# Kernel tuning notes

Hardware: AMD Instinct MI355X
Metric: run time of the kernel (lower is better)

## Reference

```python
import jax, jax.numpy as jnp
import numpy as np

N = 65536   # total sentences
B = 8192    # number of bags (ragged scopes)
C = 1024    # class_dim
R = 100     # rel_num


def setup_inputs() -> dict:
    key = jax.random.key(0)
    k1, k2, k3, k4 = jax.random.split(key, 4)
    X = jax.random.normal(k1, (N, C), jnp.float32)            # post-fc1 sentence reps
    Constraints = jax.random.normal(k2, (R, C), jnp.float32)  # post-fc2 constraint reps
    W = jax.random.normal(k3, (R, C), jnp.float32) * 0.02     # classifier weight
    b = jnp.zeros((R,), jnp.float32)                           # classifier bias
    # ragged scopes: random cut points -> contiguous [start, end) per bag
    rng = np.random.default_rng(0)
    cuts = np.sort(rng.choice(np.arange(1, N), B - 1, replace=False))
    starts = np.concatenate([[0], cuts])
    ends = np.concatenate([cuts, [N]])
    X_Scope = jnp.asarray(np.stack([starts, ends], axis=1), jnp.int32)  # [B, 2]
    X_Rel = jax.random.randint(k4, (B,), 0, R, jnp.int32)               # [B]
    return dict(X=X, Constraints=Constraints, W=W, b=b, X_Scope=X_Scope, X_Rel=X_Rel)


def reference(X, Constraints, W, b, X_Scope, X_Rel):
    n, _ = X.shape
    nb = X_Scope.shape[0]
    # map each sentence to its (contiguous) bag via scope starts
    starts = X_Scope[:, 0]
    seg = jnp.searchsorted(starts, jnp.arange(n, dtype=starts.dtype), side='right') - 1  # [N]
    # per-sentence attention logit against its bag's relation constraint
    Con = Constraints[X_Rel]                                   # [B, C]
    scores = jnp.einsum('nc,nc->n', X, Con[seg])               # [N]
    # numerically-stable per-bag softmax
    m = jax.ops.segment_max(scores, seg, num_segments=nb)      # [B]
    e = jnp.exp(scores - m[seg])                               # [N]
    denom = jax.ops.segment_sum(e, seg, num_segments=nb)       # [B]
    w = e / denom[seg]                                         # [N]
    # attention-weighted bag pooling
    bag = jax.ops.segment_sum(w[:, None] * X, seg, num_segments=nb)  # [B, C]
    # classifier (dropout is identity at eval)
    return bag @ W.T + b                                       # [B, R]
```

## Files before the change

### kernel.cpp

```cpp
#include <hip/hip_runtime.h>
#include <math.h>

#define CDIM 1024
#define RDIM 100
#define NBAGS 8192
#define RPAD 112
#define BPB 16
#define NBLK (NBAGS / BPB)

typedef float floatx4 __attribute__((ext_vector_type(4)));
typedef short bf16x8 __attribute__((ext_vector_type(8)));

__device__ __forceinline__ float dot4(float4 a, float4 b) {
    return a.x * b.x + a.y * b.y + a.z * b.z + a.w * b.w;
}

__device__ __forceinline__ unsigned short f2bf(float f) {
    unsigned int u = __builtin_bit_cast(unsigned int, f);
    u += 0x7FFFu + ((u >> 16) & 1u);
    return (unsigned short)(u >> 16);
}

#define LOADROW(D0, D1, D2, D3, ri)                                          \
    {                                                                        \
        const float4* p_ = (const float4*)(X + (size_t)(ri) * CDIM);         \
        D0 = p_[lane];       D1 = p_[lane + 64];                             \
        D2 = p_[lane + 128]; D3 = p_[lane + 192];                            \
    }

#define COMPUTE_ROW(A0, A1, A2, A3)                                          \
    {                                                                        \
        float p = dot4(A0, c0) + dot4(A1, c1) + dot4(A2, c2) + dot4(A3, c3); \
        p += __shfl_xor(p, 1);                                               \
        p += __shfl_xor(p, 2);                                               \
        p += __shfl_xor(p, 4);                                               \
        p += __shfl_xor(p, 8);                                               \
        p += __shfl_xor(p, 16);                                              \
        p += __shfl_xor(p, 32);                                              \
        const float newm = fmaxf(m, p);                                      \
        const float corr = __expf(m - newm);             \
        const float wgt  = __expf(p - newm);                                 \
        denom = fmaf(denom, corr, wgt);                                      \
        a0.x = fmaf(a0.x, corr, wgt * A0.x); a0.y = fmaf(a0.y, corr, wgt * A0.y); \
        a0.z = fmaf(a0.z, corr, wgt * A0.z); a0.w = fmaf(a0.w, corr, wgt * A0.w); \
        a1.x = fmaf(a1.x, corr, wgt * A1.x); a1.y = fmaf(a1.y, corr, wgt * A1.y); \
        a1.z = fmaf(a1.z, corr, wgt * A1.z); a1.w = fmaf(a1.w, corr, wgt * A1.w); \
        a2.x = fmaf(a2.x, corr, wgt * A2.x); a2.y = fmaf(a2.y, corr, wgt * A2.y); \
        a2.z = fmaf(a2.z, corr, wgt * A2.z); a2.w = fmaf(a2.w, corr, wgt * A2.w); \
        a3.x = fmaf(a3.x, corr, wgt * A3.x); a3.y = fmaf(a3.y, corr, wgt * A3.y); \
        a3.z = fmaf(a3.z, corr, wgt * A3.z); a3.w = fmaf(a3.w, corr, wgt * A3.w); \
        m = newm;                                                            \
    }

__global__ __launch_bounds__(256) void pw_prep(
    const float* __restrict__ W, unsigned short* __restrict__ PW)
{
    const int rr = blockIdx.x;
    const int t  = threadIdx.x;
    const int kc  = t >> 3;
    const int sub = (t >> 1) & 3;
    const int i0  = (t & 1) * 4;
    ushort4 o = {0, 0, 0, 0};
    if (rr < RDIM) {
        float4 v = *(const float4*)(W + (size_t)rr * CDIM + t * 4);
        o.x = f2bf(v.x); o.y = f2bf(v.y); o.z = f2bf(v.z); o.w = f2bf(v.w);
    }
    const int tt = rr >> 4, rl = rr & 15;
    *(ushort4*)(PW + ((size_t)(kc * 7 + tt) * 64 + sub * 16 + rl) * 8 + i0) = o;
}

__global__ __launch_bounds__(256) void fused_kernel(
    const float* __restrict__ X,
    const float* __restrict__ Constraints,
    const int* __restrict__ scope,
    const int* __restrict__ rel,
    const unsigned short* __restrict__ PW,
    const float* __restrict__ bias,
    float* __restrict__ out)
{
    __shared__ float4 mergebuf[4][256];
    __shared__ float  lds_m[4];
    __shared__ float  lds_d[4];
    __shared__ unsigned short bagsm[BPB][CDIM];

    const int lane = threadIdx.x & 63;
    const int w    = threadIdx.x >> 6;
    const int t    = threadIdx.x;
    const int bag0 = blockIdx.x * BPB;

    float4 c0, c1, c2, c3;
    {
        const float4* conp = (const float4*)(Constraints + (size_t)rel[bag0] * CDIM);
        c0 = conp[lane]; c1 = conp[lane + 64]; c2 = conp[lane + 128]; c3 = conp[lane + 192];
    }

    #pragma unroll 1
    for (int j = 0; j < BPB; ++j) {
        const int bag = bag0 + j;
        const int s = scope[2 * bag];
        const int e = scope[2 * bag + 1];

        float4 a0 = {0.f, 0.f, 0.f, 0.f};
        float4 a1 = {0.f, 0.f, 0.f, 0.f};
        float4 a2 = {0.f, 0.f, 0.f, 0.f};
        float4 a3 = {0.f, 0.f, 0.f, 0.f};
        float m = -INFINITY;
        float denom = 0.f;

        int row = s + w;
        if (row < e) {
            float4 A0, A1, A2, A3;
            float4 B0, B1, B2, B3;
            float4 C0, C1, C2, C3;

            LOADROW(A0, A1, A2, A3, row)
            if (row + 4 < e) LOADROW(B0, B1, B2, B3, row + 4)

            for (; row + 8 < e; row += 4) {
                LOADROW(C0, C1, C2, C3, row + 8)
                __builtin_amdgcn_sched_barrier(0);
                COMPUTE_ROW(A0, A1, A2, A3)
                A0 = B0; A1 = B1; A2 = B2; A3 = B3;
                B0 = C0; B1 = C1; B2 = C2; B3 = C3;
            }
            if (row + 4 < e) {
                COMPUTE_ROW(A0, A1, A2, A3)
                COMPUTE_ROW(B0, B1, B2, B3)
            } else {
                COMPUTE_ROW(A0, A1, A2, A3)
            }
        }

        float4 n0, n1, n2, n3;
        if (j + 1 < BPB) {
            const float4* conp = (const float4*)(Constraints + (size_t)rel[bag + 1] * CDIM);
            n0 = conp[lane]; n1 = conp[lane + 64]; n2 = conp[lane + 128]; n3 = conp[lane + 192];
        }

        if (lane == 0) { lds_m[w] = m; lds_d[w] = denom; }
        mergebuf[w][lane]       = a0;
        mergebuf[w][lane + 64]  = a1;
        mergebuf[w][lane + 128] = a2;
        mergebuf[w][lane + 192] = a3;
        __syncthreads();

        const float m0 = lds_m[0], m1 = lds_m[1], m2 = lds_m[2], m3 = lds_m[3];
        const float ms = fmaxf(fmaxf(m0, m1), fmaxf(m2, m3));
        const float f0 = __expf(m0 - ms);
        const float f1 = __expf(m1 - ms);
        const float f2 = __expf(m2 - ms);
        const float f3 = __expf(m3 - ms);
        const float dn = f0 * lds_d[0] + f1 * lds_d[1] + f2 * lds_d[2] + f3 * lds_d[3];
        const float inv = 1.0f / dn;

        const float4 v0 = mergebuf[0][t];
        const float4 v1 = mergebuf[1][t];
        const float4 v2 = mergebuf[2][t];
        const float4 v3 = mergebuf[3][t];
        const float ox = (f0 * v0.x + f1 * v1.x + f2 * v2.x + f3 * v3.x) * inv;
        const float oy = (f0 * v0.y + f1 * v1.y + f2 * v2.y + f3 * v3.y) * inv;
        const float oz = (f0 * v0.z + f1 * v1.z + f2 * v2.z + f3 * v3.z) * inv;
        const float ow = (f0 * v0.w + f1 * v1.w + f2 * v2.w + f3 * v3.w) * inv;

        ushort4 o;
        o.x = f2bf(ox); o.y = f2bf(oy); o.z = f2bf(oz); o.w = f2bf(ow);
        const int blk = (t >> 1) ^ (j & 7);
        *(ushort4*)((char*)&bagsm[j][0] + blk * 16 + (t & 1) * 8) = o;
        __syncthreads();

        c0 = n0; c1 = n1; c2 = n2; c3 = n3;
    }

    const int ln15 = lane & 15;
    const int kgrp = lane >> 4;
    const int tA = w, tB = w + 4;
    floatx4 accA = (floatx4){0.f, 0.f, 0.f, 0.f};
    floatx4 accB = (floatx4){0.f, 0.f, 0.f, 0.f};
    const bool hasB = (tB < 7);

    #pragma unroll 4
    for (int kc = 0; kc < CDIM / 32; ++kc) {
        const int swz = (kc * 4 + kgrp) ^ (ln15 & 7);
        const bf16x8 a = *(const bf16x8*)((const char*)&bagsm[ln15][0] + swz * 16);
        const bf16x8 bA = *(const bf16x8*)(PW + ((size_t)(kc * 7 + tA) * 64 + lane) * 8);
        accA = __builtin_amdgcn_mfma_f32_16x16x32_bf16(a, bA, accA, 0, 0, 0);
        if (hasB) {
            const bf16x8 bB = *(const bf16x8*)(PW + ((size_t)(kc * 7 + tB) * 64 + lane) * 8);
            accB = __builtin_amdgcn_mfma_f32_16x16x32_bf16(a, bB, accB, 0, 0, 0);
        }
    }

    const int mbase = kgrp * 4;
    {
        const int r = tA * 16 + ln15;
        if (r < RDIM) {
            const float bv = bias[r];
            #pragma unroll
            for (int reg = 0; reg < 4; ++reg)
                out[(size_t)(bag0 + mbase + reg) * RDIM + r] = accA[reg] + bv;
        }
    }
    if (hasB) {
        const int r = tB * 16 + ln15;
        if (r < RDIM) {
            const float bv = bias[r];
            #pragma unroll
            for (int reg = 0; reg < 4; ++reg)
                out[(size_t)(bag0 + mbase + reg) * RDIM + r] = accB[reg] + bv;
        }
    }
}

extern "C" void kernel_launch(void* const* d_in, const int* in_sizes, int n_in,
                              void* d_out, int out_size, void* d_ws, size_t ws_size,
                              hipStream_t stream) {
    const float* X    = (const float*)d_in[0];
    const float* Con  = (const float*)d_in[1];
    const float* W    = (const float*)d_in[2];
    const float* bias = (const float*)d_in[3];
    const int* scope  = (const int*)d_in[4];
    const int* rel    = (const int*)d_in[5];
    float* out = (float*)d_out;

    unsigned short* PW = (unsigned short*)d_ws;

    pw_prep<<<RPAD, 256, 0, stream>>>(W, PW);
    fused_kernel<<<NBLK, 256, 0, stream>>>(X, Con, scope, rel, PW, bias, out);
}
```

Baseline: 68.29 us.

## Assign one wave per bag with dynamic LDS work claiming, 8 waves per block

Each wave now handles a whole bag on its own and takes the next bag index through an LDS atomic counter. This removes the cross-wave softmax merge through shared memory and the two block barriers per bag. Blocks grow to 512 threads, and in the classifier stage each of 7 waves computes one 16-column MFMA tile. The trade-off is that each wave runs a serial dependency chain over its rows with a short 2-deep prefetch, so per-wave memory parallelism drops and long bags can leave the other waves idle.

```diff
diff --git a/kernel.cpp b/kernel.cpp
--- a/kernel.cpp
+++ b/kernel.cpp
@@ -7,6 +7,7 @@
 #define RPAD 112
 #define BPB 16
 #define NBLK (NBAGS / BPB)
+#define WAVES 8
 
 typedef float floatx4 __attribute__((ext_vector_type(4)));
 typedef short bf16x8 __attribute__((ext_vector_type(8)));
@@ -69,7 +70,7 @@
     *(ushort4*)(PW + ((size_t)(kc * 7 + tt) * 64 + sub * 16 + rl) * 8 + i0) = o;
 }
 
-__global__ __launch_bounds__(256) void fused_kernel(
+__global__ __launch_bounds__(512) void fused_kernel(
     const float* __restrict__ X,
     const float* __restrict__ Constraints,
     const int* __restrict__ scope,
@@ -78,27 +79,27 @@
     const float* __restrict__ bias,
     float* __restrict__ out)
 {
-    __shared__ float4 mergebuf[4][256];
-    __shared__ float  lds_m[4];
-    __shared__ float  lds_d[4];
     __shared__ unsigned short bagsm[BPB][CDIM];
+    __shared__ int claim;
 
     const int lane = threadIdx.x & 63;
     const int w    = threadIdx.x >> 6;
-    const int t    = threadIdx.x;
     const int bag0 = blockIdx.x * BPB;
 
-    float4 c0, c1, c2, c3;
-    {
-        const float4* conp = (const float4*)(Constraints + (size_t)rel[bag0] * CDIM);
-        c0 = conp[lane]; c1 = conp[lane + 64]; c2 = conp[lane + 128]; c3 = conp[lane + 192];
-    }
-
-    #pragma unroll 1
-    for (int j = 0; j < BPB; ++j) {
+    if (threadIdx.x == 0) claim = WAVES;
+    __syncthreads();
+
+    int j = w;
+    while (j < BPB) {
         const int bag = bag0 + j;
         const int s = scope[2 * bag];
         const int e = scope[2 * bag + 1];
+
+        float4 c0, c1, c2, c3;
+        {
+            const float4* conp = (const float4*)(Constraints + (size_t)rel[bag] * CDIM);
+            c0 = conp[lane]; c1 = conp[lane + 64]; c2 = conp[lane + 128]; c3 = conp[lane + 192];
+        }
 
         float4 a0 = {0.f, 0.f, 0.f, 0.f};
         float4 a1 = {0.f, 0.f, 0.f, 0.f};
@@ -107,106 +108,88 @@
         float m = -INFINITY;
         float denom = 0.f;
 
-        int row = s + w;
-        if (row < e) {
-            float4 A0, A1, A2, A3;
-            float4 B0, B1, B2, B3;
-            float4 C0, C1, C2, C3;
-
-            LOADROW(A0, A1, A2, A3, row)
-            if (row + 4 < e) LOADROW(B0, B1, B2, B3, row + 4)
-
-            for (; row + 8 < e; row += 4) {
-                LOADROW(C0, C1, C2, C3, row + 8)
-                __builtin_amdgcn_sched_barrier(0);
-                COMPUTE_ROW(A0, A1, A2, A3)
-                A0 = B0; A1 = B1; A2 = B2; A3 = B3;
-                B0 = C0; B1 = C1; B2 = C2; B3 = C3;
-            }
-            if (row + 4 < e) {
-                COMPUTE_ROW(A0, A1, A2, A3)
-                COMPUTE_ROW(B0, B1, B2, B3)
-            } else {
-                COMPUTE_ROW(A0, A1, A2, A3)
-            }
-        }
-
-        float4 n0, n1, n2, n3;
-        if (j + 1 < BPB) {
-            const float4* conp = (const float4*)(Constraints + (size_t)rel[bag + 1] * CDIM);
-            n0 = conp[lane]; n1 = conp[lane + 64]; n2 = conp[lane + 128]; n3 = conp[lane + 192];
-        }
-
-        if (lane == 0) { lds_m[w] = m; lds_d[w] = denom; }
-        mergebuf[w][lane]       = a0;
-        mergebuf[w][lane + 64]  = a1;
-        mergebuf[w][lane + 128] = a2;
-        mergebuf[w][lane + 192] = a3;
-        __syncthreads();
-
-        const float m0 = lds_m[0], m1 = lds_m[1], m2 = lds_m[2], m3 = lds_m[3];
-        const float ms = fmaxf(fmaxf(m0, m1), fmaxf(m2, m3));
-        const float f0 = __expf(m0 - ms);
-        const float f1 = __expf(m1 - ms);
-        const float f2 = __expf(m2 - ms);
-        const float f3 = __expf(m3 - ms);
-        const float dn = f0 * lds_d[0] + f1 * lds_d[1] + f2 * lds_d[2] + f3 * lds_d[3];
-        const float inv = 1.0f / dn;
-
-        const float4 v0 = mergebuf[0][t];
-        const float4 v1 = mergebuf[1][t];
-        const float4 v2 = mergebuf[2][t];
-        const float4 v3 = mergebuf[3][t];
-        const float ox = (f0 * v0.x + f1 * v1.x + f2 * v2.x + f3 * v3.x) * inv;
-        const float oy = (f0 * v0.y + f1 * v1.y + f2 * v2.y + f3 * v3.y) * inv;
-        const float oz = (f0 * v0.z + f1 * v1.z + f2 * v2.z + f3 * v3.z) * inv;
-        const float ow = (f0 * v0.w + f1 * v1.w + f2 * v2.w + f3 * v3.w) * inv;
-
-        ushort4 o;
-        o.x = f2bf(ox); o.y = f2bf(oy); o.z = f2bf(oz); o.w = f2bf(ow);
-        const int blk = (t >> 1) ^ (j & 7);
-        *(ushort4*)((char*)&bagsm[j][0] + blk * 16 + (t & 1) * 8) = o;
-        __syncthreads();
-
-        c0 = n0; c1 = n1; c2 = n2; c3 = n3;
-    }
-
-    const int ln15 = lane & 15;
-    const int kgrp = lane >> 4;
-    const int tA = w, tB = w + 4;
-    floatx4 accA = (floatx4){0.f, 0.f, 0.f, 0.f};
-    floatx4 accB = (floatx4){0.f, 0.f, 0.f, 0.f};
-    const bool hasB = (tB < 7);
-
-    #pragma unroll 4
-    for (int kc = 0; kc < CDIM / 32; ++kc) {
-        const int swz = (kc * 4 + kgrp) ^ (ln15 & 7);
-        const bf16x8 a = *(const bf16x8*)((const char*)&bagsm[ln15][0] + swz * 16);
-        const bf16x8 bA = *(const bf16x8*)(PW + ((size_t)(kc * 7 + tA) * 64 + lane) * 8);
-        accA = __builtin_amdgcn_mfma_f32_16x16x32_bf16(a, bA, accA, 0, 0, 0);
-        if (hasB) {
-            const bf16x8 bB = *(const bf16x8*)(PW + ((size_t)(kc * 7 + tB) * 64 + lane) * 8);
-            accB = __builtin_amdgcn_mfma_f32_16x16x32_bf16(a, bB, accB, 0, 0, 0);
-        }
-    }
-
-    const int mbase = kgrp * 4;
-    {
-        const int r = tA * 16 + ln15;
+        int row = s;
+        float4 A0, A1, A2, A3;
+        float4 B0, B1, B2, B3;
+        float4 C0, C1, C2, C3;
+
+        LOADROW(A0, A1, A2, A3, row)
+        if (row + 1 < e) LOADROW(B0, B1, B2, B3, row + 1)
+
+        for (; row + 2 < e; ++row) {
+            LOADROW(C0, C1, C2, C3, row + 2)
+            __builtin_amdgcn_sched_barrier(0);
+            COMPUTE_ROW(A0, A1, A2, A3)
+            A0 = B0; A1 = B1; A2 = B2; A3 = B3;
+            B0 = C0; B1 = C1; B2 = C2; B3 = C3;
+        }
+        if (row + 1 < e) {
+            COMPUTE_ROW(A0, A1, A2, A3)
+            COMPUTE_ROW(B0, B1, B2, B3)
+        } else {
+            COMPUTE_ROW(A0, A1, A2, A3)
+        }
+
+        const float inv = 1.0f / denom;
+        const int jx = j & 7;
+        {
+            ushort4 o;
+            o.x = f2bf(a0.x * inv); o.y = f2bf(a0.y * inv);
+            o.z = f2bf(a0.z * inv); o.w = f2bf(a0.w * inv);
+            const int tq = lane;
+            *(ushort4*)((char*)&bagsm[j][0] + ((tq >> 1) ^ jx) * 16 + (tq & 1) * 8) = o;
+        }
+        {
+            ushort4 o;
+            o.x = f2bf(a1.x * inv); o.y = f2bf(a1.y * inv);
+            o.z = f2bf(a1.z * inv); o.w = f2bf(a1.w * inv);
+            const int tq = lane + 64;
+            *(ushort4*)((char*)&bagsm[j][0] + ((tq >> 1) ^ jx) * 16 + (tq & 1) * 8) = o;
+        }
+        {
+            ushort4 o;
+            o.x = f2bf(a2.x * inv); o.y = f2bf(a2.y * inv);
+            o.z = f2bf(a2.z * inv); o.w = f2bf(a2.w * inv);
+            const int tq = lane + 128;
+            *(ushort4*)((char*)&bagsm[j][0] + ((tq >> 1) ^ jx) * 16 + (tq & 1) * 8) = o;
+        }
+        {
+            ushort4 o;
+            o.x = f2bf(a3.x * inv); o.y = f2bf(a3.y * inv);
+            o.z = f2bf(a3.z * inv); o.w = f2bf(a3.w * inv);
+            const int tq = lane + 192;
+            *(ushort4*)((char*)&bagsm[j][0] + ((tq >> 1) ^ jx) * 16 + (tq & 1) * 8) = o;
+        }
+
+        int nj;
+        if (lane == 0) nj = atomicAdd(&claim, 1);
+        nj = __shfl(nj, 0);
+        j = nj;
+    }
+
+    __syncthreads();
+
+    if (w < 7) {
+        const int ln15 = lane & 15;
+        const int kgrp = lane >> 4;
+        floatx4 acc = (floatx4){0.f, 0.f, 0.f, 0.f};
+        const unsigned short* bBase = PW + ((size_t)w * 64 + lane) * 8;
+
+        #pragma unroll 4
+        for (int kc = 0; kc < CDIM / 32; ++kc) {
+            const int swz = (kc * 4 + kgrp) ^ (ln15 & 7);
+            const bf16x8 a = *(const bf16x8*)((const char*)&bagsm[ln15][0] + swz * 16);
+            const bf16x8 b = *(const bf16x8*)(bBase + (size_t)kc * 7 * 512);
+            acc = __builtin_amdgcn_mfma_f32_16x16x32_bf16(a, b, acc, 0, 0, 0);
+        }
+
+        const int r = w * 16 + ln15;
         if (r < RDIM) {
             const float bv = bias[r];
+            const int mbase = kgrp * 4;
             #pragma unroll
             for (int reg = 0; reg < 4; ++reg)
-                out[(size_t)(bag0 + mbase + reg) * RDIM + r] = accA[reg] + bv;
-        }
-    }
-    if (hasB) {
-        const int r = tB * 16 + ln15;
-        if (r < RDIM) {
-            const float bv = bias[r];
-            #pragma unroll
-            for (int reg = 0; reg < 4; ++reg)
-                out[(size_t)(bag0 + mbase + reg) * RDIM + r] = accB[reg] + bv;
+                out[(size_t)(bag0 + mbase + reg) * RDIM + r] = acc[reg] + bv;
         }
     }
 }
@@ -225,5 +208,5 @@
     unsigned short* PW = (unsigned short*)d_ws;
 
     pw_prep<<<RPAD, 256, 0, stream>>>(W, PW);
-    fused_kernel<<<NBLK, 256, 0, stream>>>(X, Con, scope, rel, PW, bias, out);
-}
+    fused_kernel<<<NBLK, 512, 0, stream>>>(X, Con, scope, rel, PW, bias, out);
+}
```

Result: slower. 78.36 us, median of 2 (+14.8%).
